# Optimization experiments

Hardware: AMD Instinct MI355X
Metric: run time of the kernel (lower is better)

Reference implementation:

```python
import jax, jax.numpy as jnp
import numpy as np

K_SIZE = 7   # min_kernel_size (Parameter init value, clamped)
DIL = 2      # min_dilation (Parameter init value, clamped)


def conv2d(x, w, b):
    # x: (B, Cin, H, W), w: (Cout, Cin, kh, kw), stride 1, pad 1
    y = jax.lax.conv_general_dilated(
        x, w, window_strides=(1, 1), padding=((1, 1), (1, 1)),
        dimension_numbers=("NCHW", "OIHW", "NCHW"))
    return y + b[None, :, None, None]


def sincos_1d(length, dim, dtype):
    # standard sinusoidal encoding: (length, dim)
    half = dim // 2
    inv_freq = 1.0 / (10000.0 ** (jnp.arange(half, dtype=dtype) * 2.0 / dim))
    ang = jnp.arange(length, dtype=dtype)[:, None] * inv_freq[None, :]
    return jnp.concatenate([jnp.sin(ang), jnp.cos(ang)], axis=-1)


def positional_encoding_2d(H, W, C, dtype):
    # first C//2 channels encode height, last C//2 encode width -> (H, W, C)
    pe_h = sincos_1d(H, C // 2, dtype)  # (H, C/2)
    pe_w = sincos_1d(W, C // 2, dtype)  # (W, C/2)
    pe = jnp.concatenate([
        jnp.broadcast_to(pe_h[:, None, :], (H, W, C // 2)),
        jnp.broadcast_to(pe_w[None, :, :], (H, W, C // 2)),
    ], axis=-1)
    return pe


def na_indices(L, K, D):
    # NATTEN-style dilated neighborhood indices with border clamping.
    # Each position i attends within its dilation group g = i % D.
    i = jnp.arange(L)
    g = i % D
    r = i // D                       # rank within group
    Lg = (L - g + D - 1) // D        # group length
    start = jnp.clip(r - K // 2, 0, Lg - K)
    return g[:, None] + (start[:, None] + jnp.arange(K)[None, :]) * D  # (L, K)


def neighborhood_attention_2d(q, k, v, K, D):
    # q, k: (B, H, W, Cqk); v: (B, H, W, Cv); single head, scale = Cqk**-0.5
    B, H, W, Cqk = q.shape
    scale = jnp.asarray(Cqk, q.dtype) ** -0.5
    idx_h = na_indices(H, K, D)  # (H, K)
    idx_w = na_indices(W, K, D)  # (W, K)
    # gather neighborhood keys/values: (B, H, K, W, K, C)
    kn = k[:, idx_h][:, :, :, idx_w]
    vn = v[:, idx_h][:, :, :, idx_w]
    logits = jnp.einsum('bhwc,bhiwjc->bhwij', q * scale, kn)  # (B,H,W,K,K)
    p = jax.nn.softmax(logits.reshape(B, H, W, K * K), axis=-1)
    p = p.reshape(B, H, W, K, K)
    return jnp.einsum('bhwij,bhiwjc->bhwc', p, vn)


def setup_inputs() -> dict:
    key = jax.random.key(0)
    ks = jax.random.split(key, 4)
    B, Cin, H, W = 2, 64, 96, 96
    Ci, Co = 64, 128
    fan = Cin * 9
    s = (1.0 / fan) ** 0.5
    return {
        "x": jax.random.normal(ks[0], (B, Cin, H, W), dtype=jnp.float32),
        "wq": jax.random.normal(ks[1], (Ci, Cin, 3, 3), dtype=jnp.float32) * s,
        "bq": jnp.zeros((Ci,), dtype=jnp.float32),
        "wk": jax.random.normal(ks[2], (Ci, Cin, 3, 3), dtype=jnp.float32) * s,
        "bk": jnp.zeros((Ci,), dtype=jnp.float32),
        "wv": jax.random.normal(ks[3], (Co, Cin, 3, 3), dtype=jnp.float32) * s,
        "bv": jnp.zeros((Co,), dtype=jnp.float32),
    }


def reference(x, wq, bq, wk, bk, wv, bv):
    # Conv QKV (NCHW), then move to channels-last for attention
    q = jnp.transpose(conv2d(x, wq, bq), (0, 2, 3, 1))  # (B,H,W,Ci)
    k = jnp.transpose(conv2d(x, wk, bk), (0, 2, 3, 1))
    v = jnp.transpose(conv2d(x, wv, bv), (0, 2, 3, 1))  # (B,H,W,Co)
    B, H, W, Ci = q.shape
    pe = positional_encoding_2d(H, W, Ci, q.dtype)       # (H,W,Ci)
    pe_b = jnp.broadcast_to(pe[None], (B, H, W, Ci))
    q = jnp.concatenate([q, pe_b], axis=-1)              # (B,H,W,2*Ci)
    k = jnp.concatenate([k, pe_b], axis=-1)
    return neighborhood_attention_2d(q, k, v, K_SIZE, DIL)
```

## Files before the change

kernel.cpp:

```cpp
#include <hip/hip_runtime.h>
#include <math.h>

#define HWDIM 96
#define NPIX (HWDIM*HWDIM)
#define BATCH 2
#define CIN 64
#define CCAT 128

typedef __attribute__((ext_vector_type(8))) short bf16x8;
typedef __attribute__((ext_vector_type(4))) float f32x4;

__device__ __forceinline__ unsigned short f2bf(float f) {
    unsigned u = __builtin_bit_cast(unsigned, f);
    unsigned r = (u + 0x7FFFu + ((u >> 16) & 1u)) >> 16;
    return (unsigned short)r;
}

__global__ __launch_bounds__(256) void wb_kernel(
        const float* __restrict__ wq, const float* __restrict__ wk,
        const float* __restrict__ wv, unsigned short* __restrict__ wbT) {
    int base = blockIdx.x * 4096;
    int tid  = threadIdx.x;
    #pragma unroll
    for (int e = 0; e < 16; ++e) {
        int idx = base + e * 256 + tid;
        int t   = idx / (256 * 64);
        int rem = idx % (256 * 64);
        int co  = rem / 64;
        int ci  = rem % 64;
        float val;
        if (co < 64)        val = wq[(co * 64 + ci) * 9 + t];
        else if (co < 128)  val = wk[((co - 64) * 64 + ci) * 9 + t];
        else                val = wv[((co - 128) * 64 + ci) * 9 + t];
        wbT[(t * 256 + co) * 64 + ci] = f2bf(val);
    }
}

__global__ __launch_bounds__(256, 3) void conv_mfma(
        const float* __restrict__ x,
        const unsigned short* __restrict__ wbT,
        const float* __restrict__ bq, const float* __restrict__ bk,
        const float* __restrict__ bv,
        unsigned short* __restrict__ Qb, unsigned short* __restrict__ Kb,
        unsigned short* __restrict__ Vb) {
    __shared__ unsigned short xs[3 * 50 * 72];
    int bx      = blockIdx.x;
    int spatial = (bx & 7) * 48 + (bx >> 3);
    int b    = spatial / 192;
    int hh   = spatial % 192;
    int h    = hh >> 1;
    int w0   = (hh & 1) * 48;
    int co0  = blockIdx.y * 128;
    int tid  = threadIdx.x;

    #pragma unroll
    for (int g = 0; g < 9; ++g) {
        int i   = tid + g * 256;
        int r   = i / 768;
        int rem = i % 768;
        int ci  = rem / 12;
        int p4  = rem % 12;
        int iy  = h - 1 + r;
        float4 v = make_float4(0.f, 0.f, 0.f, 0.f);
        if (iy >= 0 && iy < HWDIM)
            v = *(const float4*)&x[((b * CIN + ci) * HWDIM + iy) * HWDIM + w0 + p4 * 4];
        int base = (r * 50 + 1 + p4 * 4) * 72 + ci;
        xs[base]       = f2bf(v.x);
        xs[base + 72]  = f2bf(v.y);
        xs[base + 144] = f2bf(v.z);
        xs[base + 216] = f2bf(v.w);
    }
    if (tid < 192) {
        #pragma unroll
        for (int e = 0; e < 2; ++e) {
            int ii   = tid + e * 192;
            int r    = ii / 128;
            int rem  = ii % 128;
            int ci   = rem >> 1;
            int side = rem & 1;
            int px   = side ? 49 : 0;
            int ix   = w0 - 1 + px;
            int iy   = h - 1 + r;
            float v = 0.f;
            if (iy >= 0 && iy < HWDIM && ix >= 0 && ix < HWDIM)
                v = x[((b * CIN + ci) * HWDIM + iy) * HWDIM + ix];
            xs[(r * 50 + px) * 72 + ci] = f2bf(v);
        }
    }
    __syncthreads();

    int lane = tid & 63;
    int wv   = tid >> 6;
    int lw   = lane & 15;
    int ksub = (lane >> 4) * 8;
    int co_t = co0 + wv * 32;

    f32x4 acc[3][2];
    #pragma unroll
    for (int m = 0; m < 3; ++m)
        #pragma unroll
        for (int n = 0; n < 2; ++n) acc[m][n] = (f32x4){0.f, 0.f, 0.f, 0.f};

    #pragma unroll
    for (int half = 0; half < 2; ++half) {
        bf16x8 Bf[9][2];
        #pragma unroll
        for (int t = 0; t < 9; ++t) {
            const unsigned short* bp = wbT + ((t * 256 + co_t + lw) * 64) + half * 32 + ksub;
            Bf[t][0] = *(const bf16x8*)(bp);
            Bf[t][1] = *(const bf16x8*)(bp + 16 * 64);
        }
        #pragma unroll
        for (int t = 0; t < 9; ++t) {
            int kh = t / 3, kw = t % 3;
            const unsigned short* ap = xs + (kh * 50 + lw + kw) * 72 + half * 32 + ksub;
            bf16x8 A0 = *(const bf16x8*)(ap);
            bf16x8 A1 = *(const bf16x8*)(ap + 16 * 72);
            bf16x8 A2 = *(const bf16x8*)(ap + 32 * 72);
            acc[0][0] = __builtin_amdgcn_mfma_f32_16x16x32_bf16(A0, Bf[t][0], acc[0][0], 0, 0, 0);
            acc[0][1] = __builtin_amdgcn_mfma_f32_16x16x32_bf16(A0, Bf[t][1], acc[0][1], 0, 0, 0);
            acc[1][0] = __builtin_amdgcn_mfma_f32_16x16x32_bf16(A1, Bf[t][0], acc[1][0], 0, 0, 0);
            acc[1][1] = __builtin_amdgcn_mfma_f32_16x16x32_bf16(A1, Bf[t][1], acc[1][1], 0, 0, 0);
            acc[2][0] = __builtin_amdgcn_mfma_f32_16x16x32_bf16(A2, Bf[t][0], acc[2][0], 0, 0, 0);
            acc[2][1] = __builtin_amdgcn_mfma_f32_16x16x32_bf16(A2, Bf[t][1], acc[2][1], 0, 0, 0);
        }
    }

    __syncthreads();
    unsigned short* xs2 = xs;
    #pragma unroll
    for (int n = 0; n < 2; ++n) {
        int co_f = co_t + n * 16 + lw;
        float bval;
        if (co_f < 64)       bval = bq[co_f];
        else if (co_f < 128) bval = bk[co_f - 64];
        else                 bval = bv[co_f - 128];
        int chl = wv * 32 + n * 16 + lw;
        #pragma unroll
        for (int m = 0; m < 3; ++m) {
            int px = m * 16 + ((lane >> 4) << 2);
            #pragma unroll
            for (int r = 0; r < 4; ++r)
                xs2[(px + r) * 136 + chl] = f2bf(acc[m][n][r] + bval);
        }
    }
    __syncthreads();

    for (int i = tid; i < 768; i += 256) {
        int px  = i >> 4;
        int seg = i & 15;
        uint4 v = *(uint4*)&xs2[px * 136 + seg * 8];
        int pix = b * NPIX + h * HWDIM + w0 + px;
        int chl = seg * 8;
        if (co0 == 0) {
            if (chl < 64) *(uint4*)&Qb[pix * CCAT + chl]        = v;
            else          *(uint4*)&Kb[pix * CCAT + (chl - 64)] = v;
        } else {
            *(uint4*)&Vb[pix * CCAT + chl] = v;
        }
    }

    if (blockIdx.y == 0) {
        for (int i = tid; i < 48 * 64; i += 256) {
            int c  = i & 63;
            int pl = i >> 6;
            int w  = w0 + pl;
            int pos = (c < 32) ? h : w;
            int j   = c & 15;
            float f   = exp2f(-(float)j * 0.83048202372184059f);
            float ang = (float)pos * f;
            float val = ((c & 16) == 0) ? __sinf(ang) : __cosf(ang);
            unsigned short bvv = f2bf(val);
            int pix = b * NPIX + h * HWDIM + w;
            Qb[pix * CCAT + 64 + c] = bvv;
            Kb[pix * CCAT + 64 + c] = bvv;
        }
    }
}

#define KPAD 136
#define LGP  114

__global__ __launch_bounds__(256, 3) void natt_mfma(
        const unsigned short* __restrict__ Qb,
        const unsigned short* __restrict__ Kb,
        const unsigned short* __restrict__ Vb,
        float* __restrict__ out) {
    __shared__ unsigned short Vt[128 * KPAD];
    __shared__ unsigned short Pb[16 * KPAD];
    __shared__ float Lg[16 * LGP];

    int bid  = blockIdx.x;
    int xcd  = bid & 7;
    int slot = bid >> 3;
    int s3   = slot % 3;
    int rest = slot / 3;
    int code = xcd * 3 + s3;
    int b  = code / 12;
    int th = code % 12;
    int tw = rest % 12;
    int gg = rest / 12;
    int gh = gg & 1;
    int gw = gg >> 1;

    int rh0 = th * 4, rw0 = tw * 4;
    int base_h = min(max(rh0 - 3, 0), 41);
    int base_w = min(max(rw0 - 3, 0), 41);
    int tid = threadIdx.x;
    int lane = tid & 63;
    int wv   = tid >> 6;
    int lw   = lane & 15;
    int ks8  = (lane >> 4) * 8;

    uint4 va[4], vb2[4];
    int   vdst[4];
    #pragma unroll
    for (int j = 0; j < 4; ++j) {
        int c = tid + j * 256;
        bool valid = (j < 3) || (tid < 32);
        int pp = c >> 4, c8 = c & 15;
        int px0 = pp * 2, px1 = px0 + 1;
        int ih0 = px0 / 10, iw0 = px0 - ih0 * 10;
        int ih1 = px1 / 10, iw1 = px1 - ih1 * 10;
        int gp0 = b * NPIX + (gh + 2 * min(base_h + ih0, 47)) * HWDIM + (gw + 2 * min(base_w + iw0, 47));
        int gp1 = b * NPIX + (gh + 2 * min(base_h + ih1, 47)) * HWDIM + (gw + 2 * min(base_w + iw1, 47));
        if (valid) {
            va[j]  = *(const uint4*)(Vb + gp0 * CCAT + c8 * 8);
            vb2[j] = *(const uint4*)(Vb + gp1 * CCAT + c8 * 8);
        }
        vdst[j] = (c8 * 8) * KPAD + (px0 ^ ((c8 & 7) << 3));
    }

    for (int i = tid; i < 1024; i += 256) {
        int row = i >> 3, sg = i & 7;
        *(uint4*)(Vt + row * KPAD + 64 + sg * 8) = (uint4){0, 0, 0, 0};
    }

    const float scale = 0.08838834764831845f;
    {
        int qi = lw >> 2, qj = lw & 3;
        const unsigned short* qsrc = Qb +
            ((b * NPIX + (gh + 2 * (rh0 + qi)) * HWDIM + (gw + 2 * (rw0 + qj))) * CCAT) + ks8;
        bf16x8 A0 = *(const bf16x8*)(qsrc);
        bf16x8 A1 = *(const bf16x8*)(qsrc + 32);
        bf16x8 A2 = *(const bf16x8*)(qsrc + 64);
        bf16x8 A3 = *(const bf16x8*)(qsrc + 96);

        #pragma unroll
        for (int tt = 0; tt < 2; ++tt) {
            int tile = wv + tt * 4;
            if (tile < 7) {
                int px = min(tile * 16 + lw, 99);
                int ih = px / 10, iw = px - ih * 10;
                const unsigned short* ksrc = Kb +
                    ((b * NPIX + (gh + 2 * min(base_h + ih, 47)) * HWDIM
                               + (gw + 2 * min(base_w + iw, 47))) * CCAT) + ks8;
                bf16x8 B0 = *(const bf16x8*)(ksrc);
                bf16x8 B1 = *(const bf16x8*)(ksrc + 32);
                bf16x8 B2 = *(const bf16x8*)(ksrc + 64);
                bf16x8 B3 = *(const bf16x8*)(ksrc + 96);
                f32x4 acc = (f32x4){0.f, 0.f, 0.f, 0.f};
                __builtin_amdgcn_s_setprio(1);
                acc = __builtin_amdgcn_mfma_f32_16x16x32_bf16(A0, B0, acc, 0, 0, 0);
                acc = __builtin_amdgcn_mfma_f32_16x16x32_bf16(A1, B1, acc, 0, 0, 0);
                acc = __builtin_amdgcn_mfma_f32_16x16x32_bf16(A2, B2, acc, 0, 0, 0);
                acc = __builtin_amdgcn_mfma_f32_16x16x32_bf16(A3, B3, acc, 0, 0, 0);
                __builtin_amdgcn_s_setprio(0);
                #pragma unroll
                for (int r = 0; r < 4; ++r) {
                    int m = (lane >> 4) * 4 + r;
                    Lg[m * LGP + tile * 16 + lw] = acc[r] * scale;
                }
            }
        }
    }
    __syncthreads();

    #pragma unroll
    for (int j = 0; j < 4; ++j) {
        bool valid = (j < 3) || (tid < 32);
        if (valid) {
            unsigned short* vp = Vt + vdst[j];
            uint4 v0 = va[j], v1 = vb2[j];
            *(unsigned*)(vp + 0 * KPAD) = (v0.x & 0xFFFFu) | (v1.x << 16);
            *(unsigned*)(vp + 1 * KPAD) = (v0.x >> 16)     | (v1.x & 0xFFFF0000u);
            *(unsigned*)(vp + 2 * KPAD) = (v0.y & 0xFFFFu) | (v1.y << 16);
            *(unsigned*)(vp + 3 * KPAD) = (v0.y >> 16)     | (v1.y & 0xFFFF0000u);
            *(unsigned*)(vp + 4 * KPAD) = (v0.z & 0xFFFFu) | (v1.z << 16);
            *(unsigned*)(vp + 5 * KPAD) = (v0.z >> 16)     | (v1.z & 0xFFFF0000u);
            *(unsigned*)(vp + 6 * KPAD) = (v0.w & 0xFFFFu) | (v1.w << 16);
            *(unsigned*)(vp + 7 * KPAD) = (v0.w >> 16)     | (v1.w & 0xFFFF0000u);
        }
    }

    int q   = tid >> 4, k16 = tid & 15;
    {
        int qi  = q >> 2, qj = q & 3;
        int rh  = rh0 + qi, rw = rw0 + qj;
        int oh  = min(max(rh - 3, 0), 41) - base_h;
        int ow  = min(max(rw - 3, 0), 41) - base_w;

        float ev[4];
        int   en[4];
        float mx = -1e30f;
        #pragma unroll
        for (int u = 0; u < 4; ++u) {
            int idx = k16 + u * 16;
            if (idx < 49) {
                int i = idx / 7, j = idx - i * 7;
                int n = (oh + i) * 10 + ow + j;
                en[u] = n;
                float l = Lg[q * LGP + n];
                ev[u] = l;
                mx = fmaxf(mx, l);
            } else { en[u] = -1; ev[u] = 0.f; }
        }
        #pragma unroll
        for (int off = 8; off > 0; off >>= 1) mx = fmaxf(mx, __shfl_xor(mx, off));
        float s = 0.f;
        #pragma unroll
        for (int u = 0; u < 4; ++u)
            if (en[u] >= 0) { ev[u] = __expf(ev[u] - mx); s += ev[u]; }
        #pragma unroll
        for (int off = 8; off > 0; off >>= 1) s += __shfl_xor(s, off);
        float rs = 1.0f / s;
        *(uint4*)(Pb + q * KPAD + k16 * 8) = (uint4){0, 0, 0, 0};
        #pragma unroll
        for (int u = 0; u < 4; ++u)
            if (en[u] >= 0) Pb[q * KPAD + en[u]] = f2bf(ev[u] * rs);
    }
    __syncthreads();

    bf16x8 A4[4];
    #pragma unroll
    for (int kk = 0; kk < 4; ++kk)
        A4[kk] = *(const bf16x8*)(Pb + lw * KPAD + kk * 32 + ks8);

    __builtin_amdgcn_s_setprio(1);
    #pragma unroll
    for (int tt = 0; tt < 2; ++tt) {
        int tile = wv * 2 + tt;
        int row  = tile * 16 + lw;
        int sw   = ((row >> 3) & 7) << 3;
        const unsigned short* vrow = Vt + row * KPAD;
        f32x4 acc = (f32x4){0.f, 0.f, 0.f, 0.f};
        #pragma unroll
        for (int kk = 0; kk < 4; ++kk) {
            bf16x8 Bf = *(const bf16x8*)(vrow + ((kk * 32 + ks8) ^ sw));
            acc = __builtin_amdgcn_mfma_f32_16x16x32_bf16(A4[kk], Bf, acc, 0, 0, 0);
        }
        int ch = row;
        #pragma unroll
        for (int r = 0; r < 4; ++r) {
            int qq = (lane >> 4) * 4 + r;
            int qi = qq >> 2, qj = qq & 3;
            int gp = b * NPIX + (gh + 2 * (rh0 + qi)) * HWDIM + (gw + 2 * (rw0 + qj));
            out[gp * CCAT + ch] = acc[r];
        }
    }
    __builtin_amdgcn_s_setprio(0);
}

extern "C" void kernel_launch(void* const* d_in, const int* in_sizes, int n_in,
                              void* d_out, int out_size, void* d_ws, size_t ws_size,
                              hipStream_t stream) {
    const float* x  = (const float*)d_in[0];
    const float* wq = (const float*)d_in[1];
    const float* bq = (const float*)d_in[2];
    const float* wk = (const float*)d_in[3];
    const float* bk = (const float*)d_in[4];
    const float* wv = (const float*)d_in[5];
    const float* bv = (const float*)d_in[6];

    unsigned short* ws = (unsigned short*)d_ws;
    unsigned short* Qb  = ws;
    unsigned short* Kb  = Qb + BATCH * NPIX * CCAT;
    unsigned short* Vb  = Kb + BATCH * NPIX * CCAT;
    unsigned short* wbT = Vb + BATCH * NPIX * CCAT;

    hipLaunchKernelGGL(wb_kernel, dim3(36), dim3(256), 0, stream,
                       wq, wk, wv, wbT);
    hipLaunchKernelGGL(conv_mfma, dim3(384, 2), dim3(256), 0, stream,
                       x, wbT, bq, bk, bv, Qb, Kb, Vb);
    hipLaunchKernelGGL(natt_mfma, dim3(1152), dim3(256), 0, stream,
                       Qb, Kb, Vb, (float*)d_out);
}
```

Measured before the change: 44.92 us.

## Fuse weight prep, conv and attention into one cooperative kernel with grid syncs

Merges the three kernel launches into a single cooperative kernel of 768 blocks that uses grid-wide syncs between weight transposition, the QKV convolution and neighborhood attention. The 1152 attention tiles are spread so that the first 384 blocks handle two tiles each. This removes the launch gaps and inter-kernel drains, at the cost of grid-barrier overhead, an uneven attention workload, and host-side occupancy queries on every call. The old three-launch path is kept as a fallback.

```diff
diff --git a/kernel.cpp b/kernel.cpp
--- a/kernel.cpp
+++ b/kernel.cpp
@@ -1,5 +1,8 @@
 #include <hip/hip_runtime.h>
+#include <hip/hip_cooperative_groups.h>
 #include <math.h>
+
+namespace cg = cooperative_groups;
 
 #define HWDIM 96
 #define NPIX (HWDIM*HWDIM)
@@ -10,48 +13,30 @@
 typedef __attribute__((ext_vector_type(8))) short bf16x8;
 typedef __attribute__((ext_vector_type(4))) float f32x4;
 
+#define KPAD 136
+#define LGP  114
+
 __device__ __forceinline__ unsigned short f2bf(float f) {
     unsigned u = __builtin_bit_cast(unsigned, f);
     unsigned r = (u + 0x7FFFu + ((u >> 16) & 1u)) >> 16;
     return (unsigned short)r;
 }
 
-__global__ __launch_bounds__(256) void wb_kernel(
-        const float* __restrict__ wq, const float* __restrict__ wk,
-        const float* __restrict__ wv, unsigned short* __restrict__ wbT) {
-    int base = blockIdx.x * 4096;
-    int tid  = threadIdx.x;
-    #pragma unroll
-    for (int e = 0; e < 16; ++e) {
-        int idx = base + e * 256 + tid;
-        int t   = idx / (256 * 64);
-        int rem = idx % (256 * 64);
-        int co  = rem / 64;
-        int ci  = rem % 64;
-        float val;
-        if (co < 64)        val = wq[(co * 64 + ci) * 9 + t];
-        else if (co < 128)  val = wk[((co - 64) * 64 + ci) * 9 + t];
-        else                val = wv[((co - 128) * 64 + ci) * 9 + t];
-        wbT[(t * 256 + co) * 64 + ci] = f2bf(val);
-    }
-}
-
-__global__ __launch_bounds__(256, 3) void conv_mfma(
-        const float* __restrict__ x,
-        const unsigned short* __restrict__ wbT,
+__device__ __forceinline__ void conv_body(
+        int bid, int tid, unsigned short* xs,
+        const float* __restrict__ x, const unsigned short* __restrict__ wbT,
         const float* __restrict__ bq, const float* __restrict__ bk,
         const float* __restrict__ bv,
         unsigned short* __restrict__ Qb, unsigned short* __restrict__ Kb,
         unsigned short* __restrict__ Vb) {
-    __shared__ unsigned short xs[3 * 50 * 72];
-    int bx      = blockIdx.x;
+    int bx      = bid % 384;
+    int by      = bid / 384;
     int spatial = (bx & 7) * 48 + (bx >> 3);
     int b    = spatial / 192;
     int hh   = spatial % 192;
     int h    = hh >> 1;
     int w0   = (hh & 1) * 48;
-    int co0  = blockIdx.y * 128;
-    int tid  = threadIdx.x;
+    int co0  = by * 128;
 
     #pragma unroll
     for (int g = 0; g < 9; ++g) {
@@ -90,10 +75,10 @@
     __syncthreads();
 
     int lane = tid & 63;
-    int wv   = tid >> 6;
+    int wid  = tid >> 6;
     int lw   = lane & 15;
     int ksub = (lane >> 4) * 8;
-    int co_t = co0 + wv * 32;
+    int co_t = co0 + wid * 32;
 
     f32x4 acc[3][2];
     #pragma unroll
@@ -135,7 +120,7 @@
         if (co_f < 64)       bval = bq[co_f];
         else if (co_f < 128) bval = bk[co_f - 64];
         else                 bval = bv[co_f - 128];
-        int chl = wv * 32 + n * 16 + lw;
+        int chl = wid * 32 + n * 16 + lw;
         #pragma unroll
         for (int m = 0; m < 3; ++m) {
             int px = m * 16 + ((lane >> 4) << 2);
@@ -160,7 +145,7 @@
         }
     }
 
-    if (blockIdx.y == 0) {
+    if (by == 0) {
         for (int i = tid; i < 48 * 64; i += 256) {
             int c  = i & 63;
             int pl = i >> 6;
@@ -178,19 +163,13 @@
     }
 }
 
-#define KPAD 136
-#define LGP  114
-
-__global__ __launch_bounds__(256, 3) void natt_mfma(
+__device__ __forceinline__ void natt_tile(
+        int bid, int tid,
+        unsigned short* Vt, unsigned short* Pb, float* Lg,
         const unsigned short* __restrict__ Qb,
         const unsigned short* __restrict__ Kb,
         const unsigned short* __restrict__ Vb,
         float* __restrict__ out) {
-    __shared__ unsigned short Vt[128 * KPAD];
-    __shared__ unsigned short Pb[16 * KPAD];
-    __shared__ float Lg[16 * LGP];
-
-    int bid  = blockIdx.x;
     int xcd  = bid & 7;
     int slot = bid >> 3;
     int s3   = slot % 3;
@@ -206,9 +185,8 @@
     int rh0 = th * 4, rw0 = tw * 4;
     int base_h = min(max(rh0 - 3, 0), 41);
     int base_w = min(max(rw0 - 3, 0), 41);
-    int tid = threadIdx.x;
     int lane = tid & 63;
-    int wv   = tid >> 6;
+    int wid  = tid >> 6;
     int lw   = lane & 15;
     int ks8  = (lane >> 4) * 8;
 
@@ -248,7 +226,7 @@
 
         #pragma unroll
         for (int tt = 0; tt < 2; ++tt) {
-            int tile = wv + tt * 4;
+            int tile = wid + tt * 4;
             if (tile < 7) {
                 int px = min(tile * 16 + lw, 99);
                 int ih = px / 10, iw = px - ih * 10;
@@ -293,7 +271,7 @@
         }
     }
 
-    int q   = tid >> 4, k16 = tid & 15;
+    int q = tid >> 4, k16 = tid & 15;
     {
         int qi  = q >> 2, qj = q & 3;
         int rh  = rh0 + qi, rw = rw0 + qj;
@@ -339,7 +317,7 @@
     __builtin_amdgcn_s_setprio(1);
     #pragma unroll
     for (int tt = 0; tt < 2; ++tt) {
-        int tile = wv * 2 + tt;
+        int tile = wid * 2 + tt;
         int row  = tile * 16 + lw;
         int sw   = ((row >> 3) & 7) << 3;
         const unsigned short* vrow = Vt + row * KPAD;
@@ -359,6 +337,90 @@
         }
     }
     __builtin_amdgcn_s_setprio(0);
+}
+
+__global__ __launch_bounds__(256, 3) void fused_all(
+        const float* __restrict__ x,
+        const float* __restrict__ wq, const float* __restrict__ wk,
+        const float* __restrict__ wv,
+        const float* __restrict__ bq, const float* __restrict__ bk,
+        const float* __restrict__ bv,
+        unsigned short* wbT, unsigned short* Qb, unsigned short* Kb,
+        unsigned short* Vb, float* out) {
+    __shared__ __align__(16) unsigned char smem[46464];
+    int bid = blockIdx.x;
+    int tid = threadIdx.x;
+
+    if (tid < 192) {
+        int idx = bid * 192 + tid;
+        int t   = idx / 16384;
+        int rem = idx % 16384;
+        int co  = rem >> 6;
+        int ci  = rem & 63;
+        float val;
+        if (co < 64)        val = wq[(co * 64 + ci) * 9 + t];
+        else if (co < 128)  val = wk[((co - 64) * 64 + ci) * 9 + t];
+        else                val = wv[((co - 128) * 64 + ci) * 9 + t];
+        wbT[(t * 256 + co) * 64 + ci] = f2bf(val);
+    }
+    __threadfence();
+    cg::this_grid().sync();
+
+    conv_body(bid, tid, (unsigned short*)smem, x, wbT, bq, bk, bv, Qb, Kb, Vb);
+    __threadfence();
+    cg::this_grid().sync();
+
+    unsigned short* Vt = (unsigned short*)smem;
+    unsigned short* Pb = (unsigned short*)(smem + 34816);
+    float*          Lg = (float*)(smem + 39168);
+    natt_tile(bid, tid, Vt, Pb, Lg, Qb, Kb, Vb, out);
+    if (bid < 384) {
+        __syncthreads();
+        natt_tile(768 + bid, tid, Vt, Pb, Lg, Qb, Kb, Vb, out);
+    }
+}
+
+__global__ __launch_bounds__(256) void wb_kernel(
+        const float* __restrict__ wq, const float* __restrict__ wk,
+        const float* __restrict__ wv, unsigned short* __restrict__ wbT) {
+    int base = blockIdx.x * 4096;
+    int tid  = threadIdx.x;
+    #pragma unroll
+    for (int e = 0; e < 16; ++e) {
+        int idx = base + e * 256 + tid;
+        int t   = idx / 16384;
+        int rem = idx % 16384;
+        int co  = rem >> 6;
+        int ci  = rem & 63;
+        float val;
+        if (co < 64)        val = wq[(co * 64 + ci) * 9 + t];
+        else if (co < 128)  val = wk[((co - 64) * 64 + ci) * 9 + t];
+        else                val = wv[((co - 128) * 64 + ci) * 9 + t];
+        wbT[(t * 256 + co) * 64 + ci] = f2bf(val);
+    }
+}
+
+__global__ __launch_bounds__(256, 3) void conv_mfma(
+        const float* __restrict__ x, const unsigned short* __restrict__ wbT,
+        const float* __restrict__ bq, const float* __restrict__ bk,
+        const float* __restrict__ bv,
+        unsigned short* __restrict__ Qb, unsigned short* __restrict__ Kb,
+        unsigned short* __restrict__ Vb) {
+    __shared__ __align__(16) unsigned short xs[10800];
+    conv_body(blockIdx.x + blockIdx.y * 384, threadIdx.x, xs,
+              x, wbT, bq, bk, bv, Qb, Kb, Vb);
+}
+
+__global__ __launch_bounds__(256, 3) void natt_mfma(
+        const unsigned short* __restrict__ Qb,
+        const unsigned short* __restrict__ Kb,
+        const unsigned short* __restrict__ Vb,
+        float* __restrict__ out) {
+    __shared__ __align__(16) unsigned char smem[46464];
+    unsigned short* Vt = (unsigned short*)smem;
+    unsigned short* Pb = (unsigned short*)(smem + 34816);
+    float*          Lg = (float*)(smem + 39168);
+    natt_tile(blockIdx.x, threadIdx.x, Vt, Pb, Lg, Qb, Kb, Vb, out);
 }
 
 extern "C" void kernel_launch(void* const* d_in, const int* in_sizes, int n_in,
@@ -372,16 +434,39 @@
     const float* wv = (const float*)d_in[5];
     const float* bv = (const float*)d_in[6];
 
-    unsigned short* ws = (unsigned short*)d_ws;
+    unsigned short* ws  = (unsigned short*)d_ws;
     unsigned short* Qb  = ws;
     unsigned short* Kb  = Qb + BATCH * NPIX * CCAT;
     unsigned short* Vb  = Kb + BATCH * NPIX * CCAT;
     unsigned short* wbT = Vb + BATCH * NPIX * CCAT;
-
-    hipLaunchKernelGGL(wb_kernel, dim3(36), dim3(256), 0, stream,
-                       wq, wk, wv, wbT);
-    hipLaunchKernelGGL(conv_mfma, dim3(384, 2), dim3(256), 0, stream,
-                       x, wbT, bq, bk, bv, Qb, Kb, Vb);
-    hipLaunchKernelGGL(natt_mfma, dim3(1152), dim3(256), 0, stream,
-                       Qb, Kb, Vb, (float*)d_out);
-}
+    float* outp = (float*)d_out;
+
+    int maxPerCU = 0;
+    hipError_t oe = hipOccupancyMaxActiveBlocksPerMultiprocessor(
+        &maxPerCU, reinterpret_cast<const void*>(&fused_all), 256, 0);
+    int dev = 0;
+    hipGetDevice(&dev);
+    int numCU = 0;
+    hipDeviceGetAttribute(&numCU, hipDeviceAttributeMultiprocessorCount, dev);
+
+    bool coop = (oe == hipSuccess) && (numCU > 0) && (maxPerCU * numCU >= 768);
+    if (coop) {
+        void* params[] = {
+            (void*)&x, (void*)&wq, (void*)&wk, (void*)&wv,
+            (void*)&bq, (void*)&bk, (void*)&bv,
+            (void*)&wbT, (void*)&Qb, (void*)&Kb, (void*)&Vb, (void*)&outp
+        };
+        hipError_t le = hipLaunchCooperativeKernel(
+            reinterpret_cast<void*>(&fused_all), dim3(768), dim3(256),
+            params, 0, stream);
+        if (le != hipSuccess) coop = false;
+    }
+    if (!coop) {
+        hipLaunchKernelGGL(wb_kernel, dim3(36), dim3(256), 0, stream,
+                           wq, wk, wv, wbT);
+        hipLaunchKernelGGL(conv_mfma, dim3(384, 2), dim3(256), 0, stream,
+                           x, wbT, bq, bk, bv, Qb, Kb, Vb);
+        hipLaunchKernelGGL(natt_mfma, dim3(1152), dim3(256), 0, stream,
+                           Qb, Kb, Vb, outp);
+    }
+}
```

After: 44.87 us. Within noise of the previous version (-0.1%).
